# Kernel tuning notes

Hardware: AMD Instinct MI355X
Metric: run time of the kernel (lower is better)

## Reference

```python
import jax, jax.numpy as jnp
import numpy as np

N = 20000          # nodes
F = 256            # num_node_features (== num_sampled_vectors)
FEAT_EMB = 63      # feat_emb_dim
EMB = FEAT_EMB + 1 # emb_dim = feat_emb_dim + val_emb_dim
CH = F * EMB       # 16384, conv1 input channels
HID = 128
OUT = 7
E = 320000         # edges


def setup_inputs() -> dict:
    key = jax.random.key(0)
    ks = jax.random.split(key, 7)
    x = jax.random.normal(ks[0], (N, F), dtype=jnp.float32)
    emb_table = jax.random.normal(ks[1], (F, FEAT_EMB), dtype=jnp.float32) * 0.02
    W1 = jax.random.normal(ks[2], (CH, HID), dtype=jnp.float32) / np.sqrt(CH)
    b1 = jnp.zeros((HID,), jnp.float32)
    W2 = jax.random.normal(ks[3], (HID, OUT), dtype=jnp.float32) / np.sqrt(HID)
    b2 = jnp.zeros((OUT,), jnp.float32)
    edge_index = jax.random.randint(ks[4], (2, E), 0, N, dtype=jnp.int32)
    return {"x": x, "emb_table": emb_table, "W1": W1, "b1": b1,
            "W2": W2, "b2": b2, "edge_index": edge_index}


def _gcn_conv(h, W, b, src, dst, norm, n):
    # PyG GCNConv: symmetric-normalized aggregation (with self loops) of x @ W, then + bias
    h = h @ W                                   # [n, out]
    msg = h[src] * norm[:, None]                # gather + edge-weight
    agg = jax.ops.segment_sum(msg, dst, num_segments=n)  # scatter-add
    return agg + b


def reference(x, emb_table, W1, b1, W2, b2, edge_index):
    n = x.shape[0]
    # StandardScaler: per-feature zero mean, unit (population) std
    mean = x.mean(axis=0)
    std = x.std(axis=0)
    std = jnp.where(std == 0, jnp.float32(1.0), std)
    xs = (x - mean) / std                       # [n, F]
    # feature embedding construction: per node, concat emb_table with its value column
    feats = jnp.concatenate(
        [jnp.broadcast_to(emb_table[None], (n, F, FEAT_EMB)), xs[:, :, None]],
        axis=-1,
    ).reshape(n, CH)                            # [n, F*EMB]
    # GCN normalization with self loops (eval mode: no dropout_adj / dropout)
    loop = jnp.arange(n, dtype=edge_index.dtype)
    src = jnp.concatenate([edge_index[0], loop])
    dst = jnp.concatenate([edge_index[1], loop])
    deg = jax.ops.segment_sum(jnp.ones_like(src, jnp.float32), dst, num_segments=n)
    dinv = jnp.where(deg > 0, jax.lax.rsqrt(deg), jnp.float32(0.0))
    norm = dinv[src] * dinv[dst]                # [E+n]
    h = jax.nn.relu(_gcn_conv(feats, W1, b1, src, dst, norm, n))
    out = _gcn_conv(h, W2, b2, src, dst, norm, n)
    return jax.nn.log_softmax(out, axis=1)
```

## Files before the change

### kernel.cpp

```cpp
#include <hip/hip_runtime.h>
#include <math.h>

#define F_   256
#define FEAT_EMB_ 63
#define HID_ 128
#define OUT_ 7
#define SLOTS 64

typedef short short8 __attribute__((ext_vector_type(8)));
typedef float f32x4 __attribute__((ext_vector_type(4)));

__device__ inline short f2bf(float f) {
    unsigned u = __float_as_uint(f);
    u += 0x7FFFu + ((u >> 16) & 1u);
    return (short)(u >> 16);
}

#define K1_CS 625
#define K1_ED 1250
#define K1_CV 256
#define K1_PK 16
#define K1_GRID (K1_CS + K1_ED + K1_CV + K1_PK)

__global__ __launch_bounds__(256) void k1_kernel(const float* __restrict__ x,
                                                 const int* __restrict__ ei,
                                                 const float* __restrict__ emb,
                                                 const float* __restrict__ W1,
                                                 float* __restrict__ colsum32,
                                                 float* __restrict__ colsq32,
                                                 int* __restrict__ deg,
                                                 int* __restrict__ adjP,
                                                 float* __restrict__ Cp32,
                                                 short* __restrict__ Wfrag, int E) {
    __shared__ float4 smem[8 * 64];
    int b = blockIdx.x;
    int t = threadIdx.x;

    if (b < K1_CS) {
        int rl = t >> 6, lane = t & 63;
        int row0 = b * 32 + rl * 8;
        float4 v[8];
#pragma unroll
        for (int i = 0; i < 8; i++)
            v[i] = *(const float4*)(x + (size_t)(row0 + i) * F_ + lane * 4);
        float4 s = make_float4(0.f, 0.f, 0.f, 0.f);
        float4 q = make_float4(0.f, 0.f, 0.f, 0.f);
#pragma unroll
        for (int i = 0; i < 8; i++) {
            s.x += v[i].x; s.y += v[i].y; s.z += v[i].z; s.w += v[i].w;
            q.x += v[i].x * v[i].x; q.y += v[i].y * v[i].y;
            q.z += v[i].z * v[i].z; q.w += v[i].w * v[i].w;
        }
        smem[rl * 64 + lane] = s;
        smem[(rl + 4) * 64 + lane] = q;
        __syncthreads();
        if (rl == 0) {
#pragma unroll
            for (int i = 1; i < 4; i++) {
                float4 a = smem[i * 64 + lane], bq = smem[(i + 4) * 64 + lane];
                s.x += a.x; s.y += a.y; s.z += a.z; s.w += a.w;
                q.x += bq.x; q.y += bq.y; q.z += bq.z; q.w += bq.w;
            }
            int buf = (b & 31) * F_;
            atomicAdd(&colsum32[buf + lane * 4 + 0], s.x);
            atomicAdd(&colsum32[buf + lane * 4 + 1], s.y);
            atomicAdd(&colsum32[buf + lane * 4 + 2], s.z);
            atomicAdd(&colsum32[buf + lane * 4 + 3], s.w);
            atomicAdd(&colsq32[buf + lane * 4 + 0], q.x);
            atomicAdd(&colsq32[buf + lane * 4 + 1], q.y);
            atomicAdd(&colsq32[buf + lane * 4 + 2], q.z);
            atomicAdd(&colsq32[buf + lane * 4 + 3], q.w);
        }
    } else if (b < K1_CS + K1_ED) {
        int e = (b - K1_CS) * 256 + t;
        if (e < E) {
            int s = ei[e];
            int d = ei[E + e];
            int pos = atomicAdd(&deg[d], 1);
            if (pos < SLOTS) adjP[(d << 6) + pos] = s;
        }
    } else if (b < K1_CS + K1_ED + K1_CV) {
        int f = b - (K1_CS + K1_ED);
        int jg = t >> 5, k4 = t & 31;
        float4 s = make_float4(0.f, 0.f, 0.f, 0.f);
        for (int j = jg; j < FEAT_EMB_; j += 8) {
            float e = emb[f * FEAT_EMB_ + j];
            float4 w = *(const float4*)(W1 + ((size_t)(f * 64 + j)) * HID_ + k4 * 4);
            s.x += e * w.x; s.y += e * w.y; s.z += e * w.z; s.w += e * w.w;
        }
        smem[jg * 32 + k4] = s;
        __syncthreads();
        if (jg == 0) {
#pragma unroll
            for (int i = 1; i < 8; i++) {
                float4 a = smem[i * 32 + k4];
                s.x += a.x; s.y += a.y; s.z += a.z; s.w += a.w;
            }
            int buf = (f & 31) * HID_;
            atomicAdd(&Cp32[buf + k4 * 4 + 0], s.x);
            atomicAdd(&Cp32[buf + k4 * 4 + 1], s.y);
            atomicAdd(&Cp32[buf + k4 * 4 + 2], s.z);
            atomicAdd(&Cp32[buf + k4 * 4 + 3], s.w);
        }
    } else {
        int pb = b - (K1_CS + K1_ED + K1_CV);
        int f0 = pb * 16;
#pragma unroll
        for (int i = 0; i < 8; i++) {
            int idx = t + i * 256;
            int f = f0 + (idx >> 7);
            int nn = idx & 127;
            float w = W1[((size_t)(f * 64 + 63)) * HID_ + nn];
            int kc = f >> 5, j = f & 7, hi2 = (f >> 3) & 3;
            int lane = hi2 * 16 + (nn & 15);
            int nt = nn >> 4;
            Wfrag[(((kc * 8 + nt) * 64 + lane) << 3) + j] = f2bf(w);
        }
    }
}

__global__ __launch_bounds__(256) void k2_kernel(const int* __restrict__ deg,
                                                 float* __restrict__ dinv,
                                                 const float* __restrict__ colsum32,
                                                 const float* __restrict__ colsq32,
                                                 float* __restrict__ mean,
                                                 float* __restrict__ rstd, int n) {
    int t = threadIdx.x;
    if (blockIdx.x < 79) {
        int i = blockIdx.x * 256 + t;
        if (i < n) dinv[i] = rsqrtf((float)deg[i] + 1.0f);
    } else {
        float s = 0.f, q = 0.f;
#pragma unroll
        for (int p = 0; p < 32; p++) {
            s += colsum32[p * F_ + t];
            q += colsq32[p * F_ + t];
        }
        float m = s / (float)n;
        float var = fmaxf(q / (float)n - m * m, 0.f);
        float sd = sqrtf(var);
        mean[t] = m;
        rstd[t] = (sd == 0.f) ? 1.f : (1.f / sd);
    }
}

__global__ __launch_bounds__(256) void mm1_kernel(const float* __restrict__ x,
                                                  const short* __restrict__ Wfrag,
                                                  const float* __restrict__ Cp32,
                                                  const float* __restrict__ mean,
                                                  const float* __restrict__ rstd,
                                                  const float* __restrict__ dinv,
                                                  unsigned short* __restrict__ g0b,
                                                  int n) {
    __shared__ float cps[HID_];
    __shared__ float4 smv[64];
    __shared__ float4 srv[64];
    int t = threadIdx.x;
    if (t < HID_) {
        float s = 0.f;
#pragma unroll
        for (int p = 0; p < 32; p++) s += Cp32[p * HID_ + t];
        cps[t] = s;
    }
    if (t < 64) {
        smv[t] = *(const float4*)(mean + t * 4);
        srv[t] = *(const float4*)(rstd + t * 4);
    }
    __syncthreads();

    int wave = t >> 6, lane = t & 63;
    int m = lane & 15;
    int hi = lane >> 4;
    int rowbase = blockIdx.x * 64 + wave * 16;
    int arow = rowbase + m;
    bool rok = arow < n;
    const float* xrow = x + (size_t)arow * F_ + hi * 8;

    f32x4 acc[8];
#pragma unroll
    for (int i = 0; i < 8; i++) acc[i] = (f32x4){0.f, 0.f, 0.f, 0.f};

#pragma unroll
    for (int kc = 0; kc < 8; kc++) {
        short8 af;
        if (rok) {
            float4 u0 = *(const float4*)(xrow + kc * 32);
            float4 u1 = *(const float4*)(xrow + kc * 32 + 4);
            int mb = kc * 8 + hi * 2;
            float4 m0 = smv[mb], m1 = smv[mb + 1];
            float4 r0 = srv[mb], r1 = srv[mb + 1];
            af[0] = f2bf((u0.x - m0.x) * r0.x);
            af[1] = f2bf((u0.y - m0.y) * r0.y);
            af[2] = f2bf((u0.z - m0.z) * r0.z);
            af[3] = f2bf((u0.w - m0.w) * r0.w);
            af[4] = f2bf((u1.x - m1.x) * r1.x);
            af[5] = f2bf((u1.y - m1.y) * r1.y);
            af[6] = f2bf((u1.z - m1.z) * r1.z);
            af[7] = f2bf((u1.w - m1.w) * r1.w);
        } else {
            af = (short8){0, 0, 0, 0, 0, 0, 0, 0};
        }
#pragma unroll
        for (int nt = 0; nt < 8; nt++) {
            short8 bf = *(const short8*)(Wfrag + (((kc * 8 + nt) * 64 + lane) << 3));
            acc[nt] = __builtin_amdgcn_mfma_f32_16x16x32_bf16(af, bf, acc[nt], 0, 0, 0);
        }
    }

    float dv[4];
#pragma unroll
    for (int r = 0; r < 4; r++) {
        int gr = rowbase + hi * 4 + r;
        dv[r] = (gr < n) ? dinv[gr] : 0.f;
    }
#pragma unroll
    for (int nt = 0; nt < 8; nt++) {
        int col = nt * 16 + m;
        float cp = cps[col];
#pragma unroll
        for (int r = 0; r < 4; r++) {
            int gr = rowbase + hi * 4 + r;
            if (gr < n)
                g0b[(size_t)gr * HID_ + col] = (unsigned short)f2bf((acc[nt][r] + cp) * dv[r]);
        }
    }
}

__global__ __launch_bounds__(256) void agg_fc2_kernel(const unsigned short* __restrict__ g0b,
                                                      const int* __restrict__ deg,
                                                      const int* __restrict__ adjP,
                                                      const float* __restrict__ dinv,
                                                      const float* __restrict__ b1,
                                                      const float* __restrict__ W2,
                                                      float* __restrict__ g2, int n) {
    int wave = threadIdx.x >> 6;
    int lane = threadIdx.x & 63;
    int d = blockIdx.x * 4 + wave;
    if (d >= n) return;

    int o0 = d << 6;
    int cnt = min(deg[d], SLOTS);
    int o1 = o0 + cnt;
    unsigned u = *(const unsigned*)(g0b + (size_t)d * HID_ + lane * 2);
    float ax = __uint_as_float(u << 16);
    float ay = __uint_as_float(u & 0xFFFF0000u);

    for (int base = o0; base < o1; base += 64) {
        int idx = (base + lane < o1) ? adjP[base + lane] : 0;
        int c2 = min(64, o1 - base);
        int j = 0;
        for (; j + 4 <= c2; j += 4) {
            int s0 = __shfl(idx, j + 0);
            int s1 = __shfl(idx, j + 1);
            int s2 = __shfl(idx, j + 2);
            int s3 = __shfl(idx, j + 3);
            unsigned u0 = *(const unsigned*)(g0b + (size_t)s0 * HID_ + lane * 2);
            unsigned u1 = *(const unsigned*)(g0b + (size_t)s1 * HID_ + lane * 2);
            unsigned u2 = *(const unsigned*)(g0b + (size_t)s2 * HID_ + lane * 2);
            unsigned u3 = *(const unsigned*)(g0b + (size_t)s3 * HID_ + lane * 2);
            ax += __uint_as_float(u0 << 16) + __uint_as_float(u1 << 16)
                + __uint_as_float(u2 << 16) + __uint_as_float(u3 << 16);
            ay += __uint_as_float(u0 & 0xFFFF0000u) + __uint_as_float(u1 & 0xFFFF0000u)
                + __uint_as_float(u2 & 0xFFFF0000u) + __uint_as_float(u3 & 0xFFFF0000u);
        }
        for (; j < c2; j++) {
            int s = __shfl(idx, j);
            unsigned uu = *(const unsigned*)(g0b + (size_t)s * HID_ + lane * 2);
            ax += __uint_as_float(uu << 16);
            ay += __uint_as_float(uu & 0xFFFF0000u);
        }
    }

    float dv = dinv[d];
    float2 bb = *(const float2*)(b1 + lane * 2);
    float h0 = fmaxf(ax * dv + bb.x, 0.f);
    float h1 = fmaxf(ay * dv + bb.y, 0.f);

    const float* w2a = W2 + (lane * 2) * OUT_;
    const float* w2b = W2 + (lane * 2 + 1) * OUT_;
    float r[OUT_];
#pragma unroll
    for (int c = 0; c < OUT_; c++) {
        float p = h0 * w2a[c] + h1 * w2b[c];
#pragma unroll
        for (int off = 32; off > 0; off >>= 1) p += __shfl_xor(p, off);
        r[c] = p;
    }
    if (lane < 8) {
        float val;
        switch (lane) {
            case 0: val = r[0]; break;
            case 1: val = r[1]; break;
            case 2: val = r[2]; break;
            case 3: val = r[3]; break;
            case 4: val = r[4]; break;
            case 5: val = r[5]; break;
            case 6: val = r[6]; break;
            default: val = 0.f; break;
        }
        g2[(size_t)d * 8 + lane] = val * dv;
    }
}

__global__ __launch_bounds__(256) void agg2_softmax_kernel(const float* __restrict__ g2,
                                                           const int* __restrict__ deg,
                                                           const int* __restrict__ adjP,
                                                           const float* __restrict__ dinv,
                                                           const float* __restrict__ b2,
                                                           float* __restrict__ out, int n) {
    int t = threadIdx.x;
    int g = t >> 3;
    int c = t & 7;
    int d = blockIdx.x * 32 + g;
    if (d >= n) return;

    int o0 = d << 6;
    int o1 = o0 + min(deg[d], SLOTS);
    float acc = g2[(size_t)d * 8 + c];
    int i = o0;
    for (; i + 2 <= o1; i += 2) {
        int s0 = adjP[i], s1 = adjP[i + 1];
        acc += g2[(size_t)s0 * 8 + c] + g2[(size_t)s1 * 8 + c];
    }
    for (; i < o1; i++) acc += g2[(size_t)adjP[i] * 8 + c];

    float z = (c < OUT_) ? (acc * dinv[d] + b2[c]) : -INFINITY;
    float m = z;
#pragma unroll
    for (int off = 4; off > 0; off >>= 1) m = fmaxf(m, __shfl_xor(m, off, 8));
    float e = (c < OUT_) ? __expf(z - m) : 0.f;
    float sum = e;
#pragma unroll
    for (int off = 4; off > 0; off >>= 1) sum += __shfl_xor(sum, off, 8);
    if (c < OUT_) out[(size_t)d * OUT_ + c] = z - m - __logf(sum);
}

extern "C" void kernel_launch(void* const* d_in, const int* in_sizes, int n_in,
                              void* d_out, int out_size, void* d_ws, size_t ws_size,
                              hipStream_t stream) {
    const float* x    = (const float*)d_in[0];
    const float* emb  = (const float*)d_in[1];
    const float* W1   = (const float*)d_in[2];
    const float* b1   = (const float*)d_in[3];
    const float* W2   = (const float*)d_in[4];
    const float* b2   = (const float*)d_in[5];
    const int*   ei   = (const int*)d_in[6];
    float* out = (float*)d_out;

    const int N = in_sizes[0] / F_;
    const int E = in_sizes[6] / 2;

    float* ws = (float*)d_ws;
    size_t o = 0;
    float* colsum32 = ws + o; o += 32 * F_;
    float* colsq32  = ws + o; o += 32 * F_;
    float* Cp32     = ws + o; o += 32 * HID_;
    int*   deg      = (int*)(ws + o); o += N;
    size_t zero_elems = o;
    float* mean     = ws + o; o += F_;
    float* rstd     = ws + o; o += F_;
    short* Wfrag    = (short*)(ws + o); o += (size_t)F_ * HID_ / 2;
    float* dinv     = ws + o; o += N;
    int*   adjP     = (int*)(ws + o); o += (size_t)N * SLOTS;
    unsigned short* g0b = (unsigned short*)(ws + o); o += (size_t)N * HID_ / 2;
    float* g2       = ws + o; o += (size_t)N * 8;

    hipMemsetAsync(ws, 0, zero_elems * sizeof(float), stream);
    k1_kernel<<<K1_GRID, 256, 0, stream>>>(x, ei, emb, W1, colsum32, colsq32,
                                           deg, adjP, Cp32, Wfrag, E);
    k2_kernel<<<80, 256, 0, stream>>>(deg, dinv, colsum32, colsq32, mean, rstd, N);
    mm1_kernel<<<(N + 63) / 64, 256, 0, stream>>>(x, Wfrag, Cp32, mean, rstd, dinv, g0b, N);
    agg_fc2_kernel<<<(N + 3) / 4, 256, 0, stream>>>(g0b, deg, adjP, dinv, b1, W2, g2, N);
    agg2_softmax_kernel<<<(N + 31) / 32, 256, 0, stream>>>(g2, deg, adjP, dinv, b2, out, N);
}
```

Measured before the change: 152.1 us.

## Fold k2 stats/dinv kernel into consumers and preload x rows in mm1

Removes the separate k2 kernel launch. Each mm1 block now reduces the column sum and sum-of-squares partials itself to get mean and rstd, and dinv is recomputed from deg wherever it is needed. The number of atomic partial buffers drops from 32 to 16 so that redundant per-block reduction is cheaper, at the cost of more atomic contention in k1. Edge blocks now handle two edges per thread, and mm1 issues all its x loads up front to overlap memory latency, which raises register pressure.

```diff
diff --git a/kernel.cpp b/kernel.cpp
--- a/kernel.cpp
+++ b/kernel.cpp
@@ -6,6 +6,7 @@
 #define HID_ 128
 #define OUT_ 7
 #define SLOTS 64
+#define NP 16
 
 typedef short short8 __attribute__((ext_vector_type(8)));
 typedef float f32x4 __attribute__((ext_vector_type(4)));
@@ -17,7 +18,7 @@
 }
 
 #define K1_CS 625
-#define K1_ED 1250
+#define K1_ED 625
 #define K1_CV 256
 #define K1_PK 16
 #define K1_GRID (K1_CS + K1_ED + K1_CV + K1_PK)
@@ -26,11 +27,11 @@
                                                  const int* __restrict__ ei,
                                                  const float* __restrict__ emb,
                                                  const float* __restrict__ W1,
-                                                 float* __restrict__ colsum32,
-                                                 float* __restrict__ colsq32,
+                                                 float* __restrict__ colsum16,
+                                                 float* __restrict__ colsq16,
                                                  int* __restrict__ deg,
                                                  int* __restrict__ adjP,
-                                                 float* __restrict__ Cp32,
+                                                 float* __restrict__ Cp16,
                                                  short* __restrict__ Wfrag, int E) {
     __shared__ float4 smem[8 * 64];
     int b = blockIdx.x;
@@ -61,23 +62,27 @@
                 s.x += a.x; s.y += a.y; s.z += a.z; s.w += a.w;
                 q.x += bq.x; q.y += bq.y; q.z += bq.z; q.w += bq.w;
             }
-            int buf = (b & 31) * F_;
-            atomicAdd(&colsum32[buf + lane * 4 + 0], s.x);
-            atomicAdd(&colsum32[buf + lane * 4 + 1], s.y);
-            atomicAdd(&colsum32[buf + lane * 4 + 2], s.z);
-            atomicAdd(&colsum32[buf + lane * 4 + 3], s.w);
-            atomicAdd(&colsq32[buf + lane * 4 + 0], q.x);
-            atomicAdd(&colsq32[buf + lane * 4 + 1], q.y);
-            atomicAdd(&colsq32[buf + lane * 4 + 2], q.z);
-            atomicAdd(&colsq32[buf + lane * 4 + 3], q.w);
+            int buf = (b & (NP - 1)) * F_;
+            atomicAdd(&colsum16[buf + lane * 4 + 0], s.x);
+            atomicAdd(&colsum16[buf + lane * 4 + 1], s.y);
+            atomicAdd(&colsum16[buf + lane * 4 + 2], s.z);
+            atomicAdd(&colsum16[buf + lane * 4 + 3], s.w);
+            atomicAdd(&colsq16[buf + lane * 4 + 0], q.x);
+            atomicAdd(&colsq16[buf + lane * 4 + 1], q.y);
+            atomicAdd(&colsq16[buf + lane * 4 + 2], q.z);
+            atomicAdd(&colsq16[buf + lane * 4 + 3], q.w);
         }
     } else if (b < K1_CS + K1_ED) {
-        int e = (b - K1_CS) * 256 + t;
-        if (e < E) {
-            int s = ei[e];
-            int d = ei[E + e];
-            int pos = atomicAdd(&deg[d], 1);
-            if (pos < SLOTS) adjP[(d << 6) + pos] = s;
+        int e0 = (b - K1_CS) * 512 + t;
+#pragma unroll
+        for (int i = 0; i < 2; i++) {
+            int e = e0 + i * 256;
+            if (e < E) {
+                int s = ei[e];
+                int d = ei[E + e];
+                int pos = atomicAdd(&deg[d], 1);
+                if (pos < SLOTS) adjP[(d << 6) + pos] = s;
+            }
         }
     } else if (b < K1_CS + K1_ED + K1_CV) {
         int f = b - (K1_CS + K1_ED);
@@ -96,11 +101,11 @@
                 float4 a = smem[i * 32 + k4];
                 s.x += a.x; s.y += a.y; s.z += a.z; s.w += a.w;
             }
-            int buf = (f & 31) * HID_;
-            atomicAdd(&Cp32[buf + k4 * 4 + 0], s.x);
-            atomicAdd(&Cp32[buf + k4 * 4 + 1], s.y);
-            atomicAdd(&Cp32[buf + k4 * 4 + 2], s.z);
-            atomicAdd(&Cp32[buf + k4 * 4 + 3], s.w);
+            int buf = (f & (NP - 1)) * HID_;
+            atomicAdd(&Cp16[buf + k4 * 4 + 0], s.x);
+            atomicAdd(&Cp16[buf + k4 * 4 + 1], s.y);
+            atomicAdd(&Cp16[buf + k4 * 4 + 2], s.z);
+            atomicAdd(&Cp16[buf + k4 * 4 + 3], s.w);
         }
     } else {
         int pb = b - (K1_CS + K1_ED + K1_CV);
@@ -119,52 +124,36 @@
     }
 }
 
-__global__ __launch_bounds__(256) void k2_kernel(const int* __restrict__ deg,
-                                                 float* __restrict__ dinv,
-                                                 const float* __restrict__ colsum32,
-                                                 const float* __restrict__ colsq32,
-                                                 float* __restrict__ mean,
-                                                 float* __restrict__ rstd, int n) {
+__global__ __launch_bounds__(256) void mm1_kernel(const float* __restrict__ x,
+                                                  const short* __restrict__ Wfrag,
+                                                  const float* __restrict__ Cp16,
+                                                  const float* __restrict__ colsum16,
+                                                  const float* __restrict__ colsq16,
+                                                  const int* __restrict__ deg,
+                                                  unsigned short* __restrict__ g0b,
+                                                  int n) {
+    __shared__ float cps[HID_];
+    __shared__ float smean[F_];
+    __shared__ float srstd[F_];
     int t = threadIdx.x;
-    if (blockIdx.x < 79) {
-        int i = blockIdx.x * 256 + t;
-        if (i < n) dinv[i] = rsqrtf((float)deg[i] + 1.0f);
-    } else {
+    {
         float s = 0.f, q = 0.f;
 #pragma unroll
-        for (int p = 0; p < 32; p++) {
-            s += colsum32[p * F_ + t];
-            q += colsq32[p * F_ + t];
+        for (int p = 0; p < NP; p++) {
+            s += colsum16[p * F_ + t];
+            q += colsq16[p * F_ + t];
         }
         float m = s / (float)n;
         float var = fmaxf(q / (float)n - m * m, 0.f);
         float sd = sqrtf(var);
-        mean[t] = m;
-        rstd[t] = (sd == 0.f) ? 1.f : (1.f / sd);
-    }
-}
-
-__global__ __launch_bounds__(256) void mm1_kernel(const float* __restrict__ x,
-                                                  const short* __restrict__ Wfrag,
-                                                  const float* __restrict__ Cp32,
-                                                  const float* __restrict__ mean,
-                                                  const float* __restrict__ rstd,
-                                                  const float* __restrict__ dinv,
-                                                  unsigned short* __restrict__ g0b,
-                                                  int n) {
-    __shared__ float cps[HID_];
-    __shared__ float4 smv[64];
-    __shared__ float4 srv[64];
-    int t = threadIdx.x;
+        smean[t] = m;
+        srstd[t] = (sd == 0.f) ? 1.f : (1.f / sd);
+    }
     if (t < HID_) {
         float s = 0.f;
 #pragma unroll
-        for (int p = 0; p < 32; p++) s += Cp32[p * HID_ + t];
+        for (int p = 0; p < NP; p++) s += Cp16[p * HID_ + t];
         cps[t] = s;
-    }
-    if (t < 64) {
-        smv[t] = *(const float4*)(mean + t * 4);
-        srv[t] = *(const float4*)(rstd + t * 4);
     }
     __syncthreads();
 
@@ -176,6 +165,18 @@
     bool rok = arow < n;
     const float* xrow = x + (size_t)arow * F_ + hi * 8;
 
+    float4 xa[8], xb[8];
+    if (rok) {
+#pragma unroll
+        for (int kc = 0; kc < 8; kc++) {
+            xa[kc] = *(const float4*)(xrow + kc * 32);
+            xb[kc] = *(const float4*)(xrow + kc * 32 + 4);
+        }
+    }
+
+    const float4* smv = (const float4*)smean;
+    const float4* srv = (const float4*)srstd;
+
     f32x4 acc[8];
 #pragma unroll
     for (int i = 0; i < 8; i++) acc[i] = (f32x4){0.f, 0.f, 0.f, 0.f};
@@ -184,19 +185,17 @@
     for (int kc = 0; kc < 8; kc++) {
         short8 af;
         if (rok) {
-            float4 u0 = *(const float4*)(xrow + kc * 32);
-            float4 u1 = *(const float4*)(xrow + kc * 32 + 4);
             int mb = kc * 8 + hi * 2;
             float4 m0 = smv[mb], m1 = smv[mb + 1];
             float4 r0 = srv[mb], r1 = srv[mb + 1];
-            af[0] = f2bf((u0.x - m0.x) * r0.x);
-            af[1] = f2bf((u0.y - m0.y) * r0.y);
-            af[2] = f2bf((u0.z - m0.z) * r0.z);
-            af[3] = f2bf((u0.w - m0.w) * r0.w);
-            af[4] = f2bf((u1.x - m1.x) * r1.x);
-            af[5] = f2bf((u1.y - m1.y) * r1.y);
-            af[6] = f2bf((u1.z - m1.z) * r1.z);
-            af[7] = f2bf((u1.w - m1.w) * r1.w);
+            af[0] = f2bf((xa[kc].x - m0.x) * r0.x);
+            af[1] = f2bf((xa[kc].y - m0.y) * r0.y);
+            af[2] = f2bf((xa[kc].z - m0.z) * r0.z);
+            af[3] = f2bf((xa[kc].w - m0.w) * r0.w);
+            af[4] = f2bf((xb[kc].x - m1.x) * r1.x);
+            af[5] = f2bf((xb[kc].y - m1.y) * r1.y);
+            af[6] = f2bf((xb[kc].z - m1.z) * r1.z);
+            af[7] = f2bf((xb[kc].w - m1.w) * r1.w);
         } else {
             af = (short8){0, 0, 0, 0, 0, 0, 0, 0};
         }
@@ -211,7 +210,7 @@
 #pragma unroll
     for (int r = 0; r < 4; r++) {
         int gr = rowbase + hi * 4 + r;
-        dv[r] = (gr < n) ? dinv[gr] : 0.f;
+        dv[r] = (gr < n) ? rsqrtf((float)deg[gr] + 1.0f) : 0.f;
     }
 #pragma unroll
     for (int nt = 0; nt < 8; nt++) {
@@ -229,7 +228,6 @@
 __global__ __launch_bounds__(256) void agg_fc2_kernel(const unsigned short* __restrict__ g0b,
                                                       const int* __restrict__ deg,
                                                       const int* __restrict__ adjP,
-                                                      const float* __restrict__ dinv,
                                                       const float* __restrict__ b1,
                                                       const float* __restrict__ W2,
                                                       float* __restrict__ g2, int n) {
@@ -238,9 +236,9 @@
     int d = blockIdx.x * 4 + wave;
     if (d >= n) return;
 
+    int dgv = deg[d];
     int o0 = d << 6;
-    int cnt = min(deg[d], SLOTS);
-    int o1 = o0 + cnt;
+    int o1 = o0 + min(dgv, SLOTS);
     unsigned u = *(const unsigned*)(g0b + (size_t)d * HID_ + lane * 2);
     float ax = __uint_as_float(u << 16);
     float ay = __uint_as_float(u & 0xFFFF0000u);
@@ -271,7 +269,7 @@
         }
     }
 
-    float dv = dinv[d];
+    float dv = rsqrtf((float)dgv + 1.0f);
     float2 bb = *(const float2*)(b1 + lane * 2);
     float h0 = fmaxf(ax * dv + bb.x, 0.f);
     float h1 = fmaxf(ay * dv + bb.y, 0.f);
@@ -305,7 +303,6 @@
 __global__ __launch_bounds__(256) void agg2_softmax_kernel(const float* __restrict__ g2,
                                                            const int* __restrict__ deg,
                                                            const int* __restrict__ adjP,
-                                                           const float* __restrict__ dinv,
                                                            const float* __restrict__ b2,
                                                            float* __restrict__ out, int n) {
     int t = threadIdx.x;
@@ -314,8 +311,9 @@
     int d = blockIdx.x * 32 + g;
     if (d >= n) return;
 
+    int dgv = deg[d];
     int o0 = d << 6;
-    int o1 = o0 + min(deg[d], SLOTS);
+    int o1 = o0 + min(dgv, SLOTS);
     float acc = g2[(size_t)d * 8 + c];
     int i = o0;
     for (; i + 2 <= o1; i += 2) {
@@ -324,7 +322,8 @@
     }
     for (; i < o1; i++) acc += g2[(size_t)adjP[i] * 8 + c];
 
-    float z = (c < OUT_) ? (acc * dinv[d] + b2[c]) : -INFINITY;
+    float dv = rsqrtf((float)dgv + 1.0f);
+    float z = (c < OUT_) ? (acc * dv + b2[c]) : -INFINITY;
     float m = z;
 #pragma unroll
     for (int off = 4; off > 0; off >>= 1) m = fmaxf(m, __shfl_xor(m, off, 8));
@@ -352,24 +351,21 @@
 
     float* ws = (float*)d_ws;
     size_t o = 0;
-    float* colsum32 = ws + o; o += 32 * F_;
-    float* colsq32  = ws + o; o += 32 * F_;
-    float* Cp32     = ws + o; o += 32 * HID_;
+    float* colsum16 = ws + o; o += NP * F_;
+    float* colsq16  = ws + o; o += NP * F_;
+    float* Cp16     = ws + o; o += NP * HID_;
     int*   deg      = (int*)(ws + o); o += N;
     size_t zero_elems = o;
-    float* mean     = ws + o; o += F_;
-    float* rstd     = ws + o; o += F_;
     short* Wfrag    = (short*)(ws + o); o += (size_t)F_ * HID_ / 2;
-    float* dinv     = ws + o; o += N;
     int*   adjP     = (int*)(ws + o); o += (size_t)N * SLOTS;
     unsigned short* g0b = (unsigned short*)(ws + o); o += (size_t)N * HID_ / 2;
     float* g2       = ws + o; o += (size_t)N * 8;
 
     hipMemsetAsync(ws, 0, zero_elems * sizeof(float), stream);
-    k1_kernel<<<K1_GRID, 256, 0, stream>>>(x, ei, emb, W1, colsum32, colsq32,
-                                           deg, adjP, Cp32, Wfrag, E);
-    k2_kernel<<<80, 256, 0, stream>>>(deg, dinv, colsum32, colsq32, mean, rstd, N);
-    mm1_kernel<<<(N + 63) / 64, 256, 0, stream>>>(x, Wfrag, Cp32, mean, rstd, dinv, g0b, N);
-    agg_fc2_kernel<<<(N + 3) / 4, 256, 0, stream>>>(g0b, deg, adjP, dinv, b1, W2, g2, N);
-    agg2_softmax_kernel<<<(N + 31) / 32, 256, 0, stream>>>(g2, deg, adjP, dinv, b2, out, N);
-}
+    k1_kernel<<<K1_GRID, 256, 0, stream>>>(x, ei, emb, W1, colsum16, colsq16,
+                                           deg, adjP, Cp16, Wfrag, E);
+    mm1_kernel<<<(N + 63) / 64, 256, 0, stream>>>(x, Wfrag, Cp16, colsum16, colsq16,
+                                                  deg, g0b, N);
+    agg_fc2_kernel<<<(N + 3) / 4, 256, 0, stream>>>(g0b, deg, adjP, b1, W2, g2, N);
+    agg2_softmax_kernel<<<(N + 31) / 32, 256, 0, stream>>>(g2, deg, adjP, b2, out, N);
+}
```

Result: faster. 147.7 us (-2.9%).
